# Kernel tuning notes

Hardware: AMD Instinct MI355X
Metric: run time of the kernel (lower is better)

The kernel has to match this reference:

```python
import jax, jax.numpy as jnp
import numpy as np

ALPHA = 0.2  # LeakyReLU negative slope
V_NODES = 7  # fixed by the module (self.B, self.A are 7x7)


def setup_inputs() -> dict:
    key = jax.random.key(0)
    k1, k2, k3 = jax.random.split(key, 3)
    N, C, T, V = 64, 256, 256, V_NODES
    F = 256  # out_features
    h = jax.random.normal(k1, (N, C, T, V), dtype=jnp.float32)
    # xavier_uniform with gain=1.414 ~ U(-b, b), b = gain*sqrt(6/(fan_in+fan_out))
    bW = 1.414 * np.sqrt(6.0 / (T + F))
    W = jax.random.uniform(k2, (T, F), dtype=jnp.float32, minval=-bW, maxval=bW)
    ba = 1.414 * np.sqrt(6.0 / (2 * F + 1))
    a = jax.random.uniform(k3, (2 * F, 1), dtype=jnp.float32, minval=-ba, maxval=ba)
    B = jnp.zeros((V, V), dtype=jnp.float32) + 1e-6
    return {"h": h, "W": W, "a": a, "B": B}


def reference(h, W, a, B):
    # h: (N, C, T, V) -> (N, V, C, T)
    h = jnp.transpose(h, (0, 3, 1, 2))
    Wh = jnp.matmul(h, W)                       # (N, V, C, F)
    F = Wh.shape[-1]
    a1 = a[:F, 0]                               # (F,)
    a2 = a[F:, 0]                               # (F,)
    # e[n,i,j,c] = a1.Wh[n,i,c,:] + a2.Wh[n,j,c,:]  (avoids (N,V,V,C,2F) materialization)
    s1 = jnp.einsum('nicf,f->nic', Wh, a1)      # (N, V, C)
    s2 = jnp.einsum('njcf,f->njc', Wh, a2)      # (N, V, C)
    e = s1[:, :, None, :] + s2[:, None, :, :]   # (N, V, V, C)
    e = jnp.where(e > 0, e, ALPHA * e)          # LeakyReLU
    att = jax.nn.softmax(e, axis=-1)            # softmax over channel dim C
    # normalized adjacency: min-max then symmetric degree normalization
    V_ = B.shape[0]
    adj = B + jnp.eye(V_, dtype=B.dtype)
    adj = (adj - jnp.min(adj)) / (jnp.max(adj) - jnp.min(adj))
    d_inv_sqrt = 1.0 / jnp.sqrt(jnp.sum(adj, axis=1))
    adj_norm = adj * d_inv_sqrt[:, None] * d_inv_sqrt[None, :]
    # diag_embed(att) matmul loop == channel-wise weighted sum over j
    h_agg = jnp.einsum('njcf,nijc->nicf', Wh, att)        # (N, V, C, F)
    out = jnp.einsum('nicf,iv->ncfv', h_agg, adj_norm)    # (N, C, F, V)
    return jax.nn.elu(out)
```

## Files before the change

### kernel.cpp

```cpp
#include <hip/hip_runtime.h>
#include <hip/hip_bf16.h>

#define LRELU_ALPHA 0.2f

typedef __attribute__((ext_vector_type(8))) short short8;
typedef __attribute__((ext_vector_type(4))) short short4v;
typedef __attribute__((ext_vector_type(4))) float f32x4;

__device__ __forceinline__ float bf2f(unsigned short u) {
  union { unsigned int i; float f; } x;
  x.i = ((unsigned int)u) << 16;
  return x.f;
}
__device__ __forceinline__ short f2bf(float f) {
  __hip_bfloat16 b = __float2bfloat16(f);
  union { __hip_bfloat16 b; short s; } u;
  u.b = b;
  return u.s;
}

__global__ __launch_bounds__(256) void k0_wt(const float* __restrict__ W,
                                             __hip_bfloat16* __restrict__ Wt) {
  int t = blockIdx.x, f = threadIdx.x;
  Wt[f * 256 + t] = __float2bfloat16(W[t * 256 + f]);
}

__global__ __launch_bounds__(64) void k0_wa(const float* __restrict__ W,
                                            const float* __restrict__ a,
                                            float* __restrict__ Wa) {
  int t = blockIdx.x, lane = threadIdx.x;
  float4 wv = *reinterpret_cast<const float4*>(W + t * 256 + lane * 4);
  float4 a1 = *reinterpret_cast<const float4*>(a + lane * 4);
  float4 a2 = *reinterpret_cast<const float4*>(a + 256 + lane * 4);
  float p1 = wv.x * a1.x + wv.y * a1.y + wv.z * a1.z + wv.w * a1.w;
  float p2 = wv.x * a2.x + wv.y * a2.y + wv.z * a2.z + wv.w * a2.w;
  #pragma unroll
  for (int off = 32; off; off >>= 1) {
    p1 += __shfl_down(p1, off);
    p2 += __shfl_down(p2, off);
  }
  if (lane == 0) { Wa[t] = p1; Wa[256 + t] = p2; }
}

__global__ __launch_bounds__(64) void k0_adj(const float* __restrict__ B,
                                             float* __restrict__ adjn) {
  int t = threadIdx.x;
  float v = 0.f;
  if (t < 49) v = B[t] + (((t / 7) == (t % 7)) ? 1.f : 0.f);
  float mn = (t < 49) ? v : 1e30f;
  float mx = (t < 49) ? v : -1e30f;
  #pragma unroll
  for (int off = 32; off; off >>= 1) {
    mn = fminf(mn, __shfl_xor(mn, off));
    mx = fmaxf(mx, __shfl_xor(mx, off));
  }
  float scaled = (v - mn) / (mx - mn);
  __shared__ float adj[49];
  __shared__ float dis[7];
  if (t < 49) adj[t] = scaled;
  __syncthreads();
  if (t < 7) {
    float s = 0.f;
    #pragma unroll
    for (int j = 0; j < 7; ++j) s += adj[t * 7 + j];
    dis[t] = 1.0f / sqrtf(s);
  }
  __syncthreads();
  if (t < 49) adjn[t] = adj[t] * dis[t / 7] * dis[t % 7];
}

__global__ __launch_bounds__(256) void k1s(const float* __restrict__ h,
                                           const float* __restrict__ Wa,
                                           float* __restrict__ s1g,
                                           float* __restrict__ s2g) {
  const int blk = blockIdx.x;
  const int n = blk >> 4, cs = blk & 15;
  const int tid = threadIdx.x;
  const int lane = tid & 63, wave = tid >> 6;
  float wa1[4], wa2[4];
  #pragma unroll
  for (int q = 0; q < 4; ++q) {
    wa1[q] = Wa[lane * 4 + q];
    wa2[q] = Wa[256 + lane * 4 + q];
  }
  #pragma unroll
  for (int ci = 0; ci < 4; ++ci) {
    int c = cs * 16 + wave * 4 + ci;
    const float4* src =
        reinterpret_cast<const float4*>(h + (size_t)(n * 256 + c) * 1792 + lane * 28);
    float4 x[7];
    #pragma unroll
    for (int i = 0; i < 7; ++i) x[i] = src[i];
    const float* xf = reinterpret_cast<const float*>(x);
    float p1[7], p2[7];
    #pragma unroll
    for (int v = 0; v < 7; ++v) { p1[v] = 0.f; p2[v] = 0.f; }
    #pragma unroll
    for (int dt = 0; dt < 4; ++dt)
      #pragma unroll
      for (int v = 0; v < 7; ++v) {
        float val = xf[dt * 7 + v];
        p1[v] += val * wa1[dt];
        p2[v] += val * wa2[dt];
      }
    #pragma unroll
    for (int v = 0; v < 7; ++v) {
      #pragma unroll
      for (int off = 32; off; off >>= 1) {
        p1[v] += __shfl_xor(p1[v], off);
        p2[v] += __shfl_xor(p2[v], off);
      }
    }
    if (lane == 0) {
      #pragma unroll
      for (int v = 0; v < 7; ++v) {
        s1g[(n * 7 + v) * 256 + c] = p1[v];
        s2g[(n * 7 + v) * 256 + c] = p2[v];
      }
    }
  }
}

__global__ __launch_bounds__(256) void k1g(const float* __restrict__ h,
                                           const __hip_bfloat16* __restrict__ Wt,
                                           __hip_bfloat16* __restrict__ Wh) {
  __shared__ short As[56 * 264];
  const int blk = blockIdx.x;
  const int n = blk >> 5, cb = blk & 31;
  const int tid = threadIdx.x;

  {
    const int c8 = tid >> 5;
    const int t0 = (tid & 31) * 8;
    const float* src = h + (size_t)((n * 256 + cb * 8 + c8)) * 1792 + t0 * 7;
    #pragma unroll
    for (int th = 0; th < 2; ++th) {
      float4 x[7];
      #pragma unroll
      for (int i = 0; i < 7; ++i)
        x[i] = reinterpret_cast<const float4*>(src + th * 28)[i];
      const float* xf = reinterpret_cast<const float*>(x);
      #pragma unroll
      for (int v = 0; v < 7; ++v) {
        short4v row;
        #pragma unroll
        for (int dt = 0; dt < 4; ++dt) row[dt] = f2bf(xf[dt * 7 + v]);
        *reinterpret_cast<short4v*>(As + (c8 * 7 + v) * 264 + t0 + th * 4) = row;
      }
    }
  }
  __syncthreads();

  const int lane = tid & 63, wave = tid >> 6;
  const int lr = lane & 15, lk = lane >> 4;
  const int f_base = wave * 64;

  f32x4 acc[4][4];
  #pragma unroll
  for (int mt = 0; mt < 4; ++mt)
    #pragma unroll
    for (int ft = 0; ft < 4; ++ft) acc[mt][ft] = (f32x4){0.f, 0.f, 0.f, 0.f};

  const short* WtS = reinterpret_cast<const short*>(Wt);

  int rowm[4];
  #pragma unroll
  for (int mt = 0; mt < 4; ++mt) {
    int m = mt * 16 + lr;
    rowm[mt] = (m < 56) ? m : 55;
  }

  #pragma unroll
  for (int kb = 0; kb < 8; ++kb) {
    short8 bfrag[4];
    #pragma unroll
    for (int ft = 0; ft < 4; ++ft)
      bfrag[ft] = *reinterpret_cast<const short8*>(
          WtS + (f_base + ft * 16 + lr) * 256 + kb * 32 + lk * 8);
    #pragma unroll
    for (int mt = 0; mt < 4; ++mt) {
      short8 afrag = *reinterpret_cast<const short8*>(
          As + rowm[mt] * 264 + kb * 32 + lk * 8);
      #pragma unroll
      for (int ft = 0; ft < 4; ++ft)
        acc[mt][ft] = __builtin_amdgcn_mfma_f32_16x16x32_bf16(afrag, bfrag[ft],
                                                              acc[mt][ft], 0, 0, 0);
    }
  }

  __syncthreads();

  #pragma unroll
  for (int mt = 0; mt < 4; ++mt) {
    #pragma unroll
    for (int j = 0; j < 4; ++j) {
      int m = mt * 16 + lk * 4 + j;
      if (m < 56) {
        #pragma unroll
        for (int ft = 0; ft < 4; ++ft)
          As[m * 264 + f_base + ft * 16 + lr] = f2bf(acc[mt][ft][j]);
      }
    }
  }
  __syncthreads();

  short* dst = reinterpret_cast<short*>(Wh) + (size_t)(n * 256 + cb * 8) * 1792;
  #pragma unroll
  for (int pass = 0; pass < 7; ++pass) {
    int r = pass * 8 + (tid >> 5);
    int col = tid & 31;
    short8 vrow = *reinterpret_cast<const short8*>(As + r * 264 + col * 8);
    *reinterpret_cast<short8*>(dst + r * 256 + col * 8) = vrow;
  }
}

__global__ __launch_bounds__(256) void k2_soft(const float* __restrict__ s1g,
                                               const float* __restrict__ s2g,
                                               float* __restrict__ att) {
  __shared__ float s1L[1792], s2L[1792];
  const int n = blockIdx.x, tid = threadIdx.x;
  for (int idx = tid; idx < 1792; idx += 256) {
    s1L[idx] = s1g[n * 1792 + idx];
    s2L[idx] = s2g[n * 1792 + idx];
  }
  __syncthreads();
  const int lane = tid & 63, wave = tid >> 6;
  for (int p = wave; p < 49; p += 4) {
    int i = p / 7, j = p - i * 7;
    float ex[4];
    float mx = -1e30f;
    #pragma unroll
    for (int q = 0; q < 4; ++q) {
      int c = lane + q * 64;
      float e = s1L[i * 256 + c] + s2L[j * 256 + c];
      e = (e > 0.f) ? e : LRELU_ALPHA * e;
      ex[q] = e;
      mx = fmaxf(mx, e);
    }
    #pragma unroll
    for (int off = 32; off; off >>= 1) mx = fmaxf(mx, __shfl_xor(mx, off));
    float sm = 0.f;
    #pragma unroll
    for (int q = 0; q < 4; ++q) {
      ex[q] = __expf(ex[q] - mx);
      sm += ex[q];
    }
    #pragma unroll
    for (int off = 32; off; off >>= 1) sm += __shfl_xor(sm, off);
    float inv = 1.0f / sm;
    #pragma unroll
    for (int q = 0; q < 4; ++q) {
      int c = lane + q * 64;
      att[((size_t)n * 256 + c) * 49 + p] = ex[q] * inv;
    }
  }
}

__global__ __launch_bounds__(256) void k3_out(const __hip_bfloat16* __restrict__ Wh,
                                              const float* __restrict__ att,
                                              const float* __restrict__ adjn,
                                              float* __restrict__ out) {
  __shared__ float attL[49], adjL[49], M[49];
  __shared__ float outL[1792];
  const int blk = blockIdx.x;
  const int n = blk >> 8, c = blk & 255;
  const int tid = threadIdx.x;
  if (tid < 49) {
    attL[tid] = att[((size_t)n * 256 + c) * 49 + tid];
    adjL[tid] = adjn[tid];
  }
  __syncthreads();
  if (tid < 49) {
    int j = tid / 7, v = tid - (tid / 7) * 7;
    float s = 0.f;
    #pragma unroll
    for (int i = 0; i < 7; ++i) s += attL[i * 7 + j] * adjL[i * 7 + v];
    M[tid] = s;
  }
  __syncthreads();
  const unsigned short* WhS = reinterpret_cast<const unsigned short*>(Wh) +
                              ((size_t)n * 256 + c) * 1792 + tid;
  float wh[7];
  #pragma unroll
  for (int j = 0; j < 7; ++j) wh[j] = bf2f(WhS[j * 256]);
  #pragma unroll
  for (int v = 0; v < 7; ++v) {
    float o = 0.f;
    #pragma unroll
    for (int j = 0; j < 7; ++j) o += wh[j] * M[j * 7 + v];
    o = (o > 0.f) ? o : (__expf(o) - 1.f);
    outL[tid * 7 + v] = o;
  }
  __syncthreads();
  float* dst = out + (size_t)(n * 256 + c) * 1792;
  for (int idx = tid; idx < 1792; idx += 256) dst[idx] = outL[idx];
}

extern "C" void kernel_launch(void* const* d_in, const int* in_sizes, int n_in,
                              void* d_out, int out_size, void* d_ws, size_t ws_size,
                              hipStream_t stream) {
  const float* h = (const float*)d_in[0];
  const float* W = (const float*)d_in[1];
  const float* a = (const float*)d_in[2];
  const float* B = (const float*)d_in[3];
  float* out = (float*)d_out;
  char* ws = (char*)d_ws;

  __hip_bfloat16* Wt = (__hip_bfloat16*)(ws + 0);
  float* adjn = (float*)(ws + 131072);
  float* Wa   = (float*)(ws + 131328);
  float* s1g  = (float*)(ws + 133376);
  float* s2g  = (float*)(ws + 592128);
  float* att  = (float*)(ws + 1050880);
  __hip_bfloat16* Wh = (__hip_bfloat16*)(ws + 4262144);

  k0_wt<<<256, 256, 0, stream>>>(W, Wt);
  k0_wa<<<256, 64, 0, stream>>>(W, a, Wa);
  k0_adj<<<1, 64, 0, stream>>>(B, adjn);
  k1s<<<1024, 256, 0, stream>>>(h, Wa, s1g, s2g);
  k1g<<<2048, 256, 0, stream>>>(h, Wt, Wh);
  k2_soft<<<64, 256, 0, stream>>>(s1g, s2g, att);
  k3_out<<<16384, 256, 0, stream>>>(Wh, att, adjn, out);
}
```

Baseline: 129.7 us.

## Fuse Wh GEMM with attention aggregation and output kernel

Merges the Wh GEMM kernel and the output aggregation kernel into one kernel. Each block computes its 8-channel Wh tile into shared memory, then builds the per-channel mixing matrices and writes ELU outputs directly. This removes the bf16 Wh intermediate written to and read back from global memory, plus one launch. In exchange, the output writes are done per thread with a 7-float stride instead of through a staged coalesced copy.

```diff
diff --git a/kernel.cpp b/kernel.cpp
--- a/kernel.cpp
+++ b/kernel.cpp
@@ -121,99 +121,6 @@
   }
 }
 
-__global__ __launch_bounds__(256) void k1g(const float* __restrict__ h,
-                                           const __hip_bfloat16* __restrict__ Wt,
-                                           __hip_bfloat16* __restrict__ Wh) {
-  __shared__ short As[56 * 264];
-  const int blk = blockIdx.x;
-  const int n = blk >> 5, cb = blk & 31;
-  const int tid = threadIdx.x;
-
-  {
-    const int c8 = tid >> 5;
-    const int t0 = (tid & 31) * 8;
-    const float* src = h + (size_t)((n * 256 + cb * 8 + c8)) * 1792 + t0 * 7;
-    #pragma unroll
-    for (int th = 0; th < 2; ++th) {
-      float4 x[7];
-      #pragma unroll
-      for (int i = 0; i < 7; ++i)
-        x[i] = reinterpret_cast<const float4*>(src + th * 28)[i];
-      const float* xf = reinterpret_cast<const float*>(x);
-      #pragma unroll
-      for (int v = 0; v < 7; ++v) {
-        short4v row;
-        #pragma unroll
-        for (int dt = 0; dt < 4; ++dt) row[dt] = f2bf(xf[dt * 7 + v]);
-        *reinterpret_cast<short4v*>(As + (c8 * 7 + v) * 264 + t0 + th * 4) = row;
-      }
-    }
-  }
-  __syncthreads();
-
-  const int lane = tid & 63, wave = tid >> 6;
-  const int lr = lane & 15, lk = lane >> 4;
-  const int f_base = wave * 64;
-
-  f32x4 acc[4][4];
-  #pragma unroll
-  for (int mt = 0; mt < 4; ++mt)
-    #pragma unroll
-    for (int ft = 0; ft < 4; ++ft) acc[mt][ft] = (f32x4){0.f, 0.f, 0.f, 0.f};
-
-  const short* WtS = reinterpret_cast<const short*>(Wt);
-
-  int rowm[4];
-  #pragma unroll
-  for (int mt = 0; mt < 4; ++mt) {
-    int m = mt * 16 + lr;
-    rowm[mt] = (m < 56) ? m : 55;
-  }
-
-  #pragma unroll
-  for (int kb = 0; kb < 8; ++kb) {
-    short8 bfrag[4];
-    #pragma unroll
-    for (int ft = 0; ft < 4; ++ft)
-      bfrag[ft] = *reinterpret_cast<const short8*>(
-          WtS + (f_base + ft * 16 + lr) * 256 + kb * 32 + lk * 8);
-    #pragma unroll
-    for (int mt = 0; mt < 4; ++mt) {
-      short8 afrag = *reinterpret_cast<const short8*>(
-          As + rowm[mt] * 264 + kb * 32 + lk * 8);
-      #pragma unroll
-      for (int ft = 0; ft < 4; ++ft)
-        acc[mt][ft] = __builtin_amdgcn_mfma_f32_16x16x32_bf16(afrag, bfrag[ft],
-                                                              acc[mt][ft], 0, 0, 0);
-    }
-  }
-
-  __syncthreads();
-
-  #pragma unroll
-  for (int mt = 0; mt < 4; ++mt) {
-    #pragma unroll
-    for (int j = 0; j < 4; ++j) {
-      int m = mt * 16 + lk * 4 + j;
-      if (m < 56) {
-        #pragma unroll
-        for (int ft = 0; ft < 4; ++ft)
-          As[m * 264 + f_base + ft * 16 + lr] = f2bf(acc[mt][ft][j]);
-      }
-    }
-  }
-  __syncthreads();
-
-  short* dst = reinterpret_cast<short*>(Wh) + (size_t)(n * 256 + cb * 8) * 1792;
-  #pragma unroll
-  for (int pass = 0; pass < 7; ++pass) {
-    int r = pass * 8 + (tid >> 5);
-    int col = tid & 31;
-    short8 vrow = *reinterpret_cast<const short8*>(As + r * 264 + col * 8);
-    *reinterpret_cast<short8*>(dst + r * 256 + col * 8) = vrow;
-  }
-}
-
 __global__ __launch_bounds__(256) void k2_soft(const float* __restrict__ s1g,
                                                const float* __restrict__ s2g,
                                                float* __restrict__ att) {
@@ -256,44 +163,126 @@
   }
 }
 
-__global__ __launch_bounds__(256) void k3_out(const __hip_bfloat16* __restrict__ Wh,
-                                              const float* __restrict__ att,
-                                              const float* __restrict__ adjn,
-                                              float* __restrict__ out) {
-  __shared__ float attL[49], adjL[49], M[49];
-  __shared__ float outL[1792];
+__global__ __launch_bounds__(256) void kC(const float* __restrict__ h,
+                                          const __hip_bfloat16* __restrict__ Wt,
+                                          const float* __restrict__ att,
+                                          const float* __restrict__ adjn,
+                                          float* __restrict__ out) {
+  __shared__ short As[56 * 264];
+  __shared__ float attL[392];
+  __shared__ float adjL[49];
+  __shared__ float Ml[392];
   const int blk = blockIdx.x;
-  const int n = blk >> 8, c = blk & 255;
+  const int n = blk >> 5, cb = blk & 31;
   const int tid = threadIdx.x;
-  if (tid < 49) {
-    attL[tid] = att[((size_t)n * 256 + c) * 49 + tid];
-    adjL[tid] = adjn[tid];
-  }
-  __syncthreads();
-  if (tid < 49) {
-    int j = tid / 7, v = tid - (tid / 7) * 7;
+
+  {
+    const int c8 = tid >> 5;
+    const int t0 = (tid & 31) * 8;
+    const float* src = h + (size_t)((n * 256 + cb * 8 + c8)) * 1792 + t0 * 7;
+    #pragma unroll
+    for (int th = 0; th < 2; ++th) {
+      float4 x[7];
+      #pragma unroll
+      for (int i = 0; i < 7; ++i)
+        x[i] = reinterpret_cast<const float4*>(src + th * 28)[i];
+      const float* xf = reinterpret_cast<const float*>(x);
+      #pragma unroll
+      for (int v = 0; v < 7; ++v) {
+        short4v row;
+        #pragma unroll
+        for (int dt = 0; dt < 4; ++dt) row[dt] = f2bf(xf[dt * 7 + v]);
+        *reinterpret_cast<short4v*>(As + (c8 * 7 + v) * 264 + t0 + th * 4) = row;
+      }
+    }
+  }
+  for (int idx = tid; idx < 392; idx += 256)
+    attL[idx] = att[(size_t)(n * 256 + cb * 8) * 49 + idx];
+  if (tid < 49) adjL[tid] = adjn[tid];
+  __syncthreads();
+
+  const int lane = tid & 63, wave = tid >> 6;
+  const int lr = lane & 15, lk = lane >> 4;
+  const int f_base = wave * 64;
+
+  f32x4 acc[4][4];
+  #pragma unroll
+  for (int mt = 0; mt < 4; ++mt)
+    #pragma unroll
+    for (int ft = 0; ft < 4; ++ft) acc[mt][ft] = (f32x4){0.f, 0.f, 0.f, 0.f};
+
+  const short* WtS = reinterpret_cast<const short*>(Wt);
+
+  int rowm[4];
+  #pragma unroll
+  for (int mt = 0; mt < 4; ++mt) {
+    int m = mt * 16 + lr;
+    rowm[mt] = (m < 56) ? m : 55;
+  }
+
+  #pragma unroll
+  for (int kb = 0; kb < 8; ++kb) {
+    short8 bfrag[4];
+    #pragma unroll
+    for (int ft = 0; ft < 4; ++ft)
+      bfrag[ft] = *reinterpret_cast<const short8*>(
+          WtS + (f_base + ft * 16 + lr) * 256 + kb * 32 + lk * 8);
+    #pragma unroll
+    for (int mt = 0; mt < 4; ++mt) {
+      short8 afrag = *reinterpret_cast<const short8*>(
+          As + rowm[mt] * 264 + kb * 32 + lk * 8);
+      #pragma unroll
+      for (int ft = 0; ft < 4; ++ft)
+        acc[mt][ft] = __builtin_amdgcn_mfma_f32_16x16x32_bf16(afrag, bfrag[ft],
+                                                              acc[mt][ft], 0, 0, 0);
+    }
+  }
+
+  for (int idx = tid; idx < 392; idx += 256) {
+    int c = idx / 49;
+    int r = idx - c * 49;
+    int j = r / 7;
+    int v = r - j * 7;
     float s = 0.f;
     #pragma unroll
-    for (int i = 0; i < 7; ++i) s += attL[i * 7 + j] * adjL[i * 7 + v];
-    M[tid] = s;
-  }
-  __syncthreads();
-  const unsigned short* WhS = reinterpret_cast<const unsigned short*>(Wh) +
-                              ((size_t)n * 256 + c) * 1792 + tid;
-  float wh[7];
-  #pragma unroll
-  for (int j = 0; j < 7; ++j) wh[j] = bf2f(WhS[j * 256]);
-  #pragma unroll
-  for (int v = 0; v < 7; ++v) {
-    float o = 0.f;
-    #pragma unroll
-    for (int j = 0; j < 7; ++j) o += wh[j] * M[j * 7 + v];
-    o = (o > 0.f) ? o : (__expf(o) - 1.f);
-    outL[tid * 7 + v] = o;
-  }
-  __syncthreads();
-  float* dst = out + (size_t)(n * 256 + c) * 1792;
-  for (int idx = tid; idx < 1792; idx += 256) dst[idx] = outL[idx];
+    for (int i = 0; i < 7; ++i) s += attL[c * 49 + i * 7 + j] * adjL[i * 7 + v];
+    Ml[idx] = s;
+  }
+
+  __syncthreads();
+
+  #pragma unroll
+  for (int mt = 0; mt < 4; ++mt) {
+    #pragma unroll
+    for (int j = 0; j < 4; ++j) {
+      int m = mt * 16 + lk * 4 + j;
+      if (m < 56) {
+        #pragma unroll
+        for (int ft = 0; ft < 4; ++ft)
+          As[m * 264 + f_base + ft * 16 + lr] = f2bf(acc[mt][ft][j]);
+      }
+    }
+  }
+  __syncthreads();
+
+  const unsigned short* AsU = reinterpret_cast<const unsigned short*>(As);
+  float* dst = out + (size_t)(n * 256 + cb * 8) * 1792 + tid * 7;
+  #pragma unroll
+  for (int c8 = 0; c8 < 8; ++c8) {
+    float wh[7];
+    #pragma unroll
+    for (int j = 0; j < 7; ++j) wh[j] = bf2f(AsU[(c8 * 7 + j) * 264 + tid]);
+    const float* Mc = Ml + c8 * 49;
+    float* dc = dst + c8 * 1792;
+    #pragma unroll
+    for (int v = 0; v < 7; ++v) {
+      float o = 0.f;
+      #pragma unroll
+      for (int j = 0; j < 7; ++j) o += wh[j] * Mc[j * 7 + v];
+      o = (o > 0.f) ? o : (__expf(o) - 1.f);
+      dc[v] = o;
+    }
+  }
 }
 
 extern "C" void kernel_launch(void* const* d_in, const int* in_sizes, int n_in,
@@ -312,13 +301,11 @@
   float* s1g  = (float*)(ws + 133376);
   float* s2g  = (float*)(ws + 592128);
   float* att  = (float*)(ws + 1050880);
-  __hip_bfloat16* Wh = (__hip_bfloat16*)(ws + 4262144);
 
   k0_wt<<<256, 256, 0, stream>>>(W, Wt);
   k0_wa<<<256, 64, 0, stream>>>(W, a, Wa);
   k0_adj<<<1, 64, 0, stream>>>(B, adjn);
   k1s<<<1024, 256, 0, stream>>>(h, Wa, s1g, s2g);
-  k1g<<<2048, 256, 0, stream>>>(h, Wt, Wh);
   k2_soft<<<64, 256, 0, stream>>>(s1g, s2g, att);
-  k3_out<<<16384, 256, 0, stream>>>(Wh, att, adjn, out);
-}
+  kC<<<2048, 256, 0, stream>>>(h, Wt, att, adjn, out);
+}
```

Measured after the change: 124.4 us. 1.04x faster.
